# Optimization experiments

Measured on AMD Instinct MI355X. Metric: run time of the kernel, lower is better.

The kernel has to match this reference:

```python
import jax, jax.numpy as jnp
import numpy as np

L = 5  # history window (init kwarg)

def _mlp(x, W1, b1, W2, b2, W3, b3):
    h = jax.nn.relu(x @ W1 + b1)
    h = jax.nn.relu(h @ W2 + b2)
    return h @ W3 + b3

def setup_inputs() -> dict:
    key = jax.random.key(0)
    ks = jax.random.split(key, 12)
    N, T1, S, D, H, E = 2000, 11, 5, 64, 256, 100000
    IN = 2 * D + 2 * L * S + 3 + 1 + 1  # 183
    return {
        "features": jax.random.normal(ks[0], (N, D), jnp.float32),
        "states": jax.random.uniform(ks[1], (N, T1, S), jnp.float32),
        "distances": jax.random.uniform(ks[2], (N, N), jnp.float32),
        "W1": jax.random.normal(ks[3], (IN, H), jnp.float32) * 0.05,
        "b1": jnp.zeros((H,), jnp.float32),
        "W2": jax.random.normal(ks[4], (H, H), jnp.float32) * 0.05,
        "b2": jnp.zeros((H,), jnp.float32),
        "W3": jax.random.normal(ks[5], (H, 3), jnp.float32) * 0.05,
        "b3": jnp.zeros((3,), jnp.float32),
        "pairs_i": jax.random.randint(ks[6], (E,), 0, N, jnp.int32),
        "pairs_j": jax.random.randint(ks[7], (E,), 0, N, jnp.int32),
        "max_timestep": 10,
    }

def reference(features, states, distances, W1, b1, W2, b2, W3, b3, pairs_i, pairs_j, max_timestep):
    T = int(max_timestep)  # static
    N, T1, S = states.shape
    E = pairs_i.shape[0]
    # --- state histories: hist[t, n] = states[n, max(0,t-L+1)..t] zero-padded, flattened to L*S
    pad = jnp.pad(states, ((0, 0), (L - 1, 0), (0, 0)))  # [N, T1+L-1, S]
    idx = jnp.arange(T + 1)[:, None] + jnp.arange(L)[None, :]  # [T+1, L]
    hist = pad[:, idx, :]  # [N, T+1, L, S]
    hist = jnp.transpose(hist, (1, 0, 2, 3)).reshape(T + 1, N, L * S)
    hist = jax.lax.stop_gradient(hist)  # original .detach()

    fi = features[pairs_i]              # [E, D]
    fj = features[pairs_j]              # [E, D]
    dist = distances[pairs_i, pairs_j][:, None]  # [E, 1]
    eye3 = jnp.eye(3, dtype=features.dtype)

    # --- t = 0: is_initial=1, dummy prev type = onehot(0); same conditional for all k_prev
    x0 = jnp.concatenate([
        fi, fj, hist[0, pairs_i], hist[0, pairs_j],
        jnp.broadcast_to(eye3[0], (E, 3)), dist, jnp.ones_like(dist)
    ], axis=-1)
    p0 = jax.nn.softmax(_mlp(x0, W1, b1, W2, b2, W3, b3), axis=-1)  # [E, 3]
    cond0 = jnp.broadcast_to(p0[:, None, :], (E, 3, 3))              # [E, 3, 3]
    m0 = p0

    # --- t >= 1: one NN call on 3 stacked prev-type branches, then forward-algo recursion
    hp_i = hist[1:, pairs_i]  # [T, E, L*S]
    hp_j = hist[1:, pairs_j]
    prev3 = jnp.broadcast_to(eye3[:, None, :], (3, E, 3))
    tail = jnp.concatenate([dist, jnp.zeros_like(dist)], axis=-1)  # [E, 2] (dist, is_initial=0)

    def step(m_prev, xs):
        hi, hj = xs
        base = jnp.concatenate([fi, fj, hi, hj], axis=-1)  # [E, 2D+2LS]
        x = jnp.concatenate([
            jnp.broadcast_to(base[None], (3, E, base.shape[-1])),
            prev3,
            jnp.broadcast_to(tail[None], (3, E, 2)),
        ], axis=-1)  # [3, E, IN]
        probs = jax.nn.softmax(_mlp(x, W1, b1, W2, b2, W3, b3), axis=-1)  # [3, E, 3]
        cond = jnp.transpose(probs, (1, 0, 2))  # [E, k_prev, k_next]
        m = jnp.einsum('ek,ekn->en', m_prev, cond)
        return m, (cond, m)

    _, (conds, margs) = jax.lax.scan(step, m0, (hp_i, hp_j))
    conditionals = jnp.concatenate([cond0[None], conds], axis=0)  # [T+1, E, 3, 3]
    marginals = jnp.concatenate([m0[None], margs], axis=0)        # [T+1, E, 3]
    return conditionals, marginals
```

## Files before the change

### kernel.cpp

```cpp
#include <hip/hip_runtime.h>
#include <hip/hip_bf16.h>
#include <math.h>

#define D_F   64
#define IN_F  183
#define KS1   6
#define KS2   8
#define HID   256
#define HPITCH 264
#define BM    64
#define BLK   512

typedef unsigned short u16;
typedef __attribute__((ext_vector_type(8))) short bf16x8;
typedef __attribute__((ext_vector_type(4))) float f32x4;

__device__ __forceinline__ u16 f2bf(float v) {
    __hip_bfloat16 h = __float2bfloat16(v);
    u16 u; __builtin_memcpy(&u, &h, 2); return u;
}

__global__ void pack_w_kernel(const float* __restrict__ W, u16* __restrict__ Wp,
                              int K, int KSs)
{
    int g = blockIdx.x * 256 + threadIdx.x;
    int total = 16 * KSs * 64;
    if (g >= total) return;
    int lane = g & 63;
    int ks   = (g >> 6) % KSs;
    int ct   = (g >> 6) / KSs;
    int col  = ct * 16 + (lane & 15);
    int kb   = ks * 32 + 8 * (lane >> 4);
    u16 out[8];
    #pragma unroll
    for (int j = 0; j < 8; ++j) {
        int k = kb + j;
        out[j] = f2bf((k < K) ? W[(size_t)k * HID + col] : 0.0f);
    }
    *(bf16x8*)(Wp + (size_t)g * 8) = *(const bf16x8*)out;
}

__global__ void pack_w3_kernel(const float* __restrict__ W3, u16* __restrict__ W3p)
{
    int g = blockIdx.x * 256 + threadIdx.x;
    if (g >= KS2 * 64) return;
    int lane = g & 63;
    int ks   = g >> 6;
    int n    = lane & 15;
    int kb   = ks * 32 + 8 * (lane >> 4);
    u16 out[8];
    #pragma unroll
    for (int j = 0; j < 8; ++j)
        out[j] = f2bf((n < 3) ? W3[(size_t)(kb + j) * 3 + n] : 0.0f);
    *(bf16x8*)(W3p + (size_t)g * 8) = *(const bf16x8*)out;
}

__global__ __launch_bounds__(BLK)
void mfp_mlp_mfma(const float* __restrict__ features,
                  const float* __restrict__ states,
                  const float* __restrict__ distances,
                  const float* __restrict__ W1,
                  const u16* __restrict__ W1p, const float* __restrict__ b1,
                  const u16* __restrict__ W2p, const float* __restrict__ b2,
                  const u16* __restrict__ W3p, const float* __restrict__ b3,
                  const int* __restrict__ pairs_i, const int* __restrict__ pairs_j,
                  float* __restrict__ cond,
                  int N, int T1s, int E, int T)
{
    extern __shared__ char smem[];
    u16* hsA = (u16*)smem;
    __shared__ int   s_pi[BM], s_pj[BM], s_e[BM], s_val[BM];
    __shared__ float s_dist[BM];

    const int tid = threadIdx.x;
    const int t   = blockIdx.y;
    const int nk  = (t == 0) ? 1 : 3;

    if (tid < BM) {
        int pe = blockIdx.x * BM + tid;
        int valid = (pe < E) ? 1 : 0;
        int e = valid ? pe : 0;
        int pi = pairs_i[e], pj = pairs_j[e];
        s_e[tid] = e; s_val[tid] = valid; s_pi[tid] = pi; s_pj[tid] = pj;
        s_dist[tid] = distances[(long long)pi * N + pj];
    }
    __syncthreads();

    u16* xs = hsA;
    for (int idx = tid; idx < BM * 32; idx += BLK) {
        int m = idx >> 5;
        int q = idx & 31;
        int src = (q < 16) ? s_pi[m] : s_pj[m];
        int c4  = (q & 15) * 4;
        float4 f = *(const float4*)&features[(size_t)src * D_F + c4];
        int c = ((q < 16) ? 0 : 64) + c4;
        ushort4 o;
        o.x = f2bf(f.x); o.y = f2bf(f.y); o.z = f2bf(f.z); o.w = f2bf(f.w);
        *(ushort4*)(xs + m * HPITCH + c) = o;
    }
    for (int idx = tid; idx < BM * 64; idx += BLK) {
        int m = idx >> 6;
        int c = 128 + (idx & 63);
        float v;
        if (c < 178) {
            int cc = c - 128;
            int row = (cc < 25) ? s_pi[m] : s_pj[m];
            int c2  = (cc < 25) ? cc : (cc - 25);
            int l = c2 / 5;
            int s = c2 - l * 5;
            int tau = t - 4 + l;
            v = (tau >= 0) ? states[((size_t)row * T1s + tau) * 5 + s] : 0.0f;
        } else if (c == 181) {
            v = s_dist[m];
        } else if (c == 182) {
            v = (t == 0) ? 1.0f : 0.0f;
        } else {
            v = 0.0f;
        }
        xs[m * HPITCH + c] = f2bf(v);
    }
    __syncthreads();

    const int lane = tid & 63;
    const int w    = tid >> 6;
    const int lr   = lane & 15;
    const int lg   = lane >> 4;

    f32x4 acc1[2][4];
    #pragma unroll
    for (int a = 0; a < 2; ++a)
        #pragma unroll
        for (int b = 0; b < 4; ++b)
            acc1[a][b] = (f32x4){0.f, 0.f, 0.f, 0.f};

    for (int ks = 0; ks < KS1; ++ks) {
        bf16x8 wfr[2];
        #pragma unroll
        for (int mtl = 0; mtl < 2; ++mtl)
            wfr[mtl] = *(const bf16x8*)(W1p + (((size_t)(2 * w + mtl) * KS1 + ks) * 64 + lane) * 8);
        bf16x8 xfr[4];
        #pragma unroll
        for (int nt = 0; nt < 4; ++nt)
            xfr[nt] = *(const bf16x8*)(xs + (nt * 16 + lr) * HPITCH + ks * 32 + 8 * lg);
        #pragma unroll
        for (int mtl = 0; mtl < 2; ++mtl)
            #pragma unroll
            for (int nt = 0; nt < 4; ++nt)
                acc1[mtl][nt] = __builtin_amdgcn_mfma_f32_16x16x32_bf16(wfr[mtl], xfr[nt], acc1[mtl][nt], 0, 0, 0);
    }

    f32x4 b1q[2], b2q[2];
    #pragma unroll
    for (int mtl = 0; mtl < 2; ++mtl) {
        int h0 = 16 * (2 * w + mtl) + 4 * lg;
        b1q[mtl] = *(const f32x4*)&b1[h0];
        b2q[mtl] = *(const f32x4*)&b2[h0];
    }
    const float b30 = b3[0], b31 = b3[1], b32 = b3[2];

    for (int k = 0; k < nk; ++k) {
        f32x4 ohq[2];
        #pragma unroll
        for (int mtl = 0; mtl < 2; ++mtl)
            ohq[mtl] = *(const f32x4*)&W1[(size_t)(178 + k) * HID + 16 * (2 * w + mtl) + 4 * lg];

        __syncthreads();

        #pragma unroll
        for (int mtl = 0; mtl < 2; ++mtl)
            #pragma unroll
            for (int nt = 0; nt < 4; ++nt) {
                ushort4 p;
                p.x = f2bf(fmaxf(acc1[mtl][nt][0] + b1q[mtl][0] + ohq[mtl][0], 0.0f));
                p.y = f2bf(fmaxf(acc1[mtl][nt][1] + b1q[mtl][1] + ohq[mtl][1], 0.0f));
                p.z = f2bf(fmaxf(acc1[mtl][nt][2] + b1q[mtl][2] + ohq[mtl][2], 0.0f));
                p.w = f2bf(fmaxf(acc1[mtl][nt][3] + b1q[mtl][3] + ohq[mtl][3], 0.0f));
                *(ushort4*)(hsA + (nt * 16 + lr) * HPITCH + 16 * (2 * w + mtl) + 4 * lg) = p;
            }
        __syncthreads();

        f32x4 acc2[2][4];
        #pragma unroll
        for (int a = 0; a < 2; ++a)
            #pragma unroll
            for (int b = 0; b < 4; ++b)
                acc2[a][b] = (f32x4){0.f, 0.f, 0.f, 0.f};

        for (int ks = 0; ks < KS2; ++ks) {
            bf16x8 wfr[2];
            #pragma unroll
            for (int mtl = 0; mtl < 2; ++mtl)
                wfr[mtl] = *(const bf16x8*)(W2p + (((size_t)(2 * w + mtl) * KS2 + ks) * 64 + lane) * 8);
            bf16x8 hfr[4];
            #pragma unroll
            for (int nt = 0; nt < 4; ++nt)
                hfr[nt] = *(const bf16x8*)(hsA + (nt * 16 + lr) * HPITCH + ks * 32 + 8 * lg);
            #pragma unroll
            for (int mtl = 0; mtl < 2; ++mtl)
                #pragma unroll
                for (int nt = 0; nt < 4; ++nt)
                    acc2[mtl][nt] = __builtin_amdgcn_mfma_f32_16x16x32_bf16(wfr[mtl], hfr[nt], acc2[mtl][nt], 0, 0, 0);
        }
        __syncthreads();

        #pragma unroll
        for (int mtl = 0; mtl < 2; ++mtl)
            #pragma unroll
            for (int nt = 0; nt < 4; ++nt) {
                ushort4 p;
                p.x = f2bf(fmaxf(acc2[mtl][nt][0] + b2q[mtl][0], 0.0f));
                p.y = f2bf(fmaxf(acc2[mtl][nt][1] + b2q[mtl][1], 0.0f));
                p.z = f2bf(fmaxf(acc2[mtl][nt][2] + b2q[mtl][2], 0.0f));
                p.w = f2bf(fmaxf(acc2[mtl][nt][3] + b2q[mtl][3], 0.0f));
                *(ushort4*)(hsA + (nt * 16 + lr) * HPITCH + 16 * (2 * w + mtl) + 4 * lg) = p;
            }
        __syncthreads();

        if (w < 4) {
            f32x4 acc3 = (f32x4){0.f, 0.f, 0.f, 0.f};
            for (int ks = 0; ks < KS2; ++ks) {
                bf16x8 hfr = *(const bf16x8*)(hsA + (w * 16 + lr) * HPITCH + ks * 32 + 8 * lg);
                bf16x8 wfr = *(const bf16x8*)(W3p + ((size_t)(ks * 64 + lane)) * 8);
                acc3 = __builtin_amdgcn_mfma_f32_16x16x32_bf16(wfr, hfr, acc3, 0, 0, 0);
            }
            int m = 16 * w + lr;
            if (lg == 0 && s_val[m]) {
                float l0 = acc3[0] + b30;
                float l1 = acc3[1] + b31;
                float l2 = acc3[2] + b32;
                float mx = fmaxf(l0, fmaxf(l1, l2));
                float e0 = expf(l0 - mx), e1 = expf(l1 - mx), e2 = expf(l2 - mx);
                float inv = 1.0f / (e0 + e1 + e2);
                float p0 = e0 * inv, p1 = e1 * inv, p2 = e2 * inv;
                size_t base = ((size_t)t * E + s_e[m]) * 9;
                if (t == 0) {
                    #pragma unroll
                    for (int kb = 0; kb < 3; ++kb) {
                        cond[base + kb * 3 + 0] = p0;
                        cond[base + kb * 3 + 1] = p1;
                        cond[base + kb * 3 + 2] = p2;
                    }
                } else {
                    cond[base + k * 3 + 0] = p0;
                    cond[base + k * 3 + 1] = p1;
                    cond[base + k * 3 + 2] = p2;
                }
            }
        }
    }
}

__global__ __launch_bounds__(256)
void mfp_marg_kernel(const float* __restrict__ cond,
                     float* __restrict__ marg,
                     int E, int T)
{
    int e = blockIdx.x * 256 + threadIdx.x;
    if (e >= E) return;
    const float* c0 = &cond[(size_t)e * 9];
    float m0 = c0[0], m1 = c0[1], m2 = c0[2];
    marg[(size_t)e * 3 + 0] = m0;
    marg[(size_t)e * 3 + 1] = m1;
    marg[(size_t)e * 3 + 2] = m2;
    for (int t = 1; t <= T; ++t) {
        const float* c9 = &cond[((size_t)t * E + e) * 9];
        float n0 = m0 * c9[0] + m1 * c9[3] + m2 * c9[6];
        float n1 = m0 * c9[1] + m1 * c9[4] + m2 * c9[7];
        float n2 = m0 * c9[2] + m1 * c9[5] + m2 * c9[8];
        m0 = n0; m1 = n1; m2 = n2;
        float* mo = &marg[((size_t)t * E + e) * 3];
        mo[0] = m0; mo[1] = m1; mo[2] = m2;
    }
}

extern "C" void kernel_launch(void* const* d_in, const int* in_sizes, int n_in,
                              void* d_out, int out_size, void* d_ws, size_t ws_size,
                              hipStream_t stream) {
    const float* features  = (const float*)d_in[0];
    const float* states    = (const float*)d_in[1];
    const float* distances = (const float*)d_in[2];
    const float* W1 = (const float*)d_in[3];
    const float* b1 = (const float*)d_in[4];
    const float* W2 = (const float*)d_in[5];
    const float* b2 = (const float*)d_in[6];
    const float* W3 = (const float*)d_in[7];
    const float* b3 = (const float*)d_in[8];
    const int* pairs_i = (const int*)d_in[9];
    const int* pairs_j = (const int*)d_in[10];

    const int N   = in_sizes[0] / D_F;
    const int T1s = in_sizes[1] / (N * 5);
    const int E   = in_sizes[9];
    const int T   = out_size / (12 * E) - 1;

    float* cond = (float*)d_out;
    float* marg = (float*)d_out + (size_t)(T + 1) * E * 9;

    u16* W1p = (u16*)d_ws;
    u16* W2p = W1p + 16 * KS1 * 64 * 8;
    u16* W3p = W2p + 16 * KS2 * 64 * 8;

    {
        int g1 = 16 * KS1 * 64;
        int g2 = 16 * KS2 * 64;
        int g3 = KS2 * 64;
        pack_w_kernel<<<(g1 + 255) / 256, 256, 0, stream>>>(W1, W1p, IN_F, KS1);
        pack_w_kernel<<<(g2 + 255) / 256, 256, 0, stream>>>(W2, W2p, HID, KS2);
        pack_w3_kernel<<<(g3 + 255) / 256, 256, 0, stream>>>(W3, W3p);
    }

    dim3 grid((E + BM - 1) / BM, T + 1);
    const size_t lds_bytes = (size_t)BM * HPITCH * sizeof(u16);

    mfp_mlp_mfma<<<grid, BLK, lds_bytes, stream>>>(
        features, states, distances, W1, W1p, b1, W2p, b2, W3p, b3,
        pairs_i, pairs_j, cond, N, T1s, E, T);

    mfp_marg_kernel<<<(E + 255) / 256, 256, 0, stream>>>(cond, marg, E, T);
}
```

Baseline: 886.8 us.

## Double-buffer layer-1 activations and split layer-2 output buffer to cut barriers

```diff
diff --git a/kernel.cpp b/kernel.cpp
--- a/kernel.cpp
+++ b/kernel.cpp
@@ -28,8 +28,8 @@
     if (g >= total) return;
     int lane = g & 63;
     int ks   = (g >> 6) % KSs;
-    int ct   = (g >> 6) / KSs;
-    int col  = ct * 16 + (lane & 15);
+    int mt   = (g >> 6) / KSs;
+    int col  = mt * 16 + (lane & 15);
     int kb   = ks * 32 + 8 * (lane >> 4);
     u16 out[8];
     #pragma unroll
@@ -68,7 +68,9 @@
                   int N, int T1s, int E, int T)
 {
     extern __shared__ char smem[];
-    u16* hsA = (u16*)smem;
+    u16* buf0 = (u16*)smem;
+    u16* buf1 = buf0 + BM * HPITCH;
+    u16* hsB  = buf1 + BM * HPITCH;
     __shared__ int   s_pi[BM], s_pj[BM], s_e[BM], s_val[BM];
     __shared__ float s_dist[BM];
 
@@ -86,7 +88,7 @@
     }
     __syncthreads();
 
-    u16* xs = hsA;
+    u16* xs = buf0;
     for (int idx = tid; idx < BM * 32; idx += BLK) {
         int m = idx >> 5;
         int q = idx & 31;
@@ -158,26 +160,44 @@
     }
     const float b30 = b3[0], b31 = b3[1], b32 = b3[2];
 
+    __syncthreads();
+
+    #pragma unroll
+    for (int mtl = 0; mtl < 2; ++mtl) {
+        int h0 = 16 * (2 * w + mtl) + 4 * lg;
+        f32x4 ohq = *(const f32x4*)&W1[(size_t)178 * HID + h0];
+        #pragma unroll
+        for (int nt = 0; nt < 4; ++nt) {
+            ushort4 p;
+            p.x = f2bf(fmaxf(acc1[mtl][nt][0] + b1q[mtl][0] + ohq[0], 0.0f));
+            p.y = f2bf(fmaxf(acc1[mtl][nt][1] + b1q[mtl][1] + ohq[1], 0.0f));
+            p.z = f2bf(fmaxf(acc1[mtl][nt][2] + b1q[mtl][2] + ohq[2], 0.0f));
+            p.w = f2bf(fmaxf(acc1[mtl][nt][3] + b1q[mtl][3] + ohq[3], 0.0f));
+            *(ushort4*)(buf1 + (nt * 16 + lr) * HPITCH + h0) = p;
+        }
+    }
+    __syncthreads();
+
     for (int k = 0; k < nk; ++k) {
-        f32x4 ohq[2];
-        #pragma unroll
-        for (int mtl = 0; mtl < 2; ++mtl)
-            ohq[mtl] = *(const f32x4*)&W1[(size_t)(178 + k) * HID + 16 * (2 * w + mtl) + 4 * lg];
-
-        __syncthreads();
-
-        #pragma unroll
-        for (int mtl = 0; mtl < 2; ++mtl)
-            #pragma unroll
-            for (int nt = 0; nt < 4; ++nt) {
-                ushort4 p;
-                p.x = f2bf(fmaxf(acc1[mtl][nt][0] + b1q[mtl][0] + ohq[mtl][0], 0.0f));
-                p.y = f2bf(fmaxf(acc1[mtl][nt][1] + b1q[mtl][1] + ohq[mtl][1], 0.0f));
-                p.z = f2bf(fmaxf(acc1[mtl][nt][2] + b1q[mtl][2] + ohq[mtl][2], 0.0f));
-                p.w = f2bf(fmaxf(acc1[mtl][nt][3] + b1q[mtl][3] + ohq[mtl][3], 0.0f));
-                *(ushort4*)(hsA + (nt * 16 + lr) * HPITCH + 16 * (2 * w + mtl) + 4 * lg) = p;
+        u16* cur = (k & 1) ? buf0 : buf1;
+        u16* nxt = (k & 1) ? buf1 : buf0;
+
+        if (k + 1 < nk) {
+            #pragma unroll
+            for (int mtl = 0; mtl < 2; ++mtl) {
+                int h0 = 16 * (2 * w + mtl) + 4 * lg;
+                f32x4 ohq = *(const f32x4*)&W1[(size_t)(178 + k + 1) * HID + h0];
+                #pragma unroll
+                for (int nt = 0; nt < 4; ++nt) {
+                    ushort4 p;
+                    p.x = f2bf(fmaxf(acc1[mtl][nt][0] + b1q[mtl][0] + ohq[0], 0.0f));
+                    p.y = f2bf(fmaxf(acc1[mtl][nt][1] + b1q[mtl][1] + ohq[1], 0.0f));
+                    p.z = f2bf(fmaxf(acc1[mtl][nt][2] + b1q[mtl][2] + ohq[2], 0.0f));
+                    p.w = f2bf(fmaxf(acc1[mtl][nt][3] + b1q[mtl][3] + ohq[3], 0.0f));
+                    *(ushort4*)(nxt + (nt * 16 + lr) * HPITCH + h0) = p;
+                }
             }
-        __syncthreads();
+        }
 
         f32x4 acc2[2][4];
         #pragma unroll
@@ -194,17 +214,17 @@
             bf16x8 hfr[4];
             #pragma unroll
             for (int nt = 0; nt < 4; ++nt)
-                hfr[nt] = *(const bf16x8*)(hsA + (nt * 16 + lr) * HPITCH + ks * 32 + 8 * lg);
+                hfr[nt] = *(const bf16x8*)(cur + (nt * 16 + lr) * HPITCH + ks * 32 + 8 * lg);
             #pragma unroll
             for (int mtl = 0; mtl < 2; ++mtl)
                 #pragma unroll
                 for (int nt = 0; nt < 4; ++nt)
                     acc2[mtl][nt] = __builtin_amdgcn_mfma_f32_16x16x32_bf16(wfr[mtl], hfr[nt], acc2[mtl][nt], 0, 0, 0);
         }
-        __syncthreads();
-
-        #pragma unroll
-        for (int mtl = 0; mtl < 2; ++mtl)
+
+        #pragma unroll
+        for (int mtl = 0; mtl < 2; ++mtl) {
+            int h0 = 16 * (2 * w + mtl) + 4 * lg;
             #pragma unroll
             for (int nt = 0; nt < 4; ++nt) {
                 ushort4 p;
@@ -212,14 +232,15 @@
                 p.y = f2bf(fmaxf(acc2[mtl][nt][1] + b2q[mtl][1], 0.0f));
                 p.z = f2bf(fmaxf(acc2[mtl][nt][2] + b2q[mtl][2], 0.0f));
                 p.w = f2bf(fmaxf(acc2[mtl][nt][3] + b2q[mtl][3], 0.0f));
-                *(ushort4*)(hsA + (nt * 16 + lr) * HPITCH + 16 * (2 * w + mtl) + 4 * lg) = p;
+                *(ushort4*)(hsB + (nt * 16 + lr) * HPITCH + h0) = p;
             }
+        }
         __syncthreads();
 
         if (w < 4) {
             f32x4 acc3 = (f32x4){0.f, 0.f, 0.f, 0.f};
             for (int ks = 0; ks < KS2; ++ks) {
-                bf16x8 hfr = *(const bf16x8*)(hsA + (w * 16 + lr) * HPITCH + ks * 32 + 8 * lg);
+                bf16x8 hfr = *(const bf16x8*)(hsB + (w * 16 + lr) * HPITCH + ks * 32 + 8 * lg);
                 bf16x8 wfr = *(const bf16x8*)(W3p + ((size_t)(ks * 64 + lane)) * 8);
                 acc3 = __builtin_amdgcn_mfma_f32_16x16x32_bf16(wfr, hfr, acc3, 0, 0, 0);
             }
@@ -247,6 +268,7 @@
                 }
             }
         }
+        __syncthreads();
     }
 }
 
@@ -310,7 +332,7 @@
     }
 
     dim3 grid((E + BM - 1) / BM, T + 1);
-    const size_t lds_bytes = (size_t)BM * HPITCH * sizeof(u16);
+    const size_t lds_bytes = (size_t)3 * BM * HPITCH * sizeof(u16);
 
     mfp_mlp_mfma<<<grid, BLK, lds_bytes, stream>>>(
         features, states, distances, W1, W1p, b1, W2p, b2, W3p, b3,
```

Result: faster. 868.8 us (-2.0%).
